# Kernel tuning notes

Measured on AMD Instinct MI355X. Metric: run time of the kernel, lower is better.

The kernel has to match this reference:

```python
import jax, jax.numpy as jnp
import numpy as np

B, C, H, W = 32, 1024, 28, 28
TEXT_DIM = 768
ATTN_DIM = 256
REDUCTION = 16
RED = max(1, C // REDUCTION)


def setup_inputs() -> dict:
    key = jax.random.key(0)
    ks = jax.random.split(key, 8)
    x = jax.random.normal(ks[0], (B, C, H, W), dtype=jnp.float32)
    text_feat = jax.random.normal(ks[1], (B, TEXT_DIM), dtype=jnp.float32)
    # ChannelAttention shared MLP (Linear weights, torch layout [out, in], no bias)
    w1 = jax.random.normal(ks[2], (RED, C), dtype=jnp.float32) * (1.0 / np.sqrt(C))
    w2 = jax.random.normal(ks[3], (C, RED), dtype=jnp.float32) * (1.0 / np.sqrt(RED))
    # TextGuidedSpatialAttention projections
    wq = jax.random.normal(ks[4], (ATTN_DIM, TEXT_DIM), dtype=jnp.float32) * 0.001
    wk = jax.random.normal(ks[5], (ATTN_DIM, C), dtype=jnp.float32) * np.sqrt(2.0 / ATTN_DIM)
    wv = jax.random.normal(ks[6], (ATTN_DIM, C), dtype=jnp.float32) * np.sqrt(2.0 / ATTN_DIM)
    wo = jax.random.normal(ks[7], (1, ATTN_DIM), dtype=jnp.float32) * np.sqrt(2.0)
    return {"x": x, "text_feat": text_feat, "w1": w1, "w2": w2,
            "wq": wq, "wk": wk, "wv": wv, "wo": wo}


def _forward(x, text_feat, w1, w2, wq, wk, wv, wo):
    b, c, h, w = x.shape
    # ----- Channel attention -----
    avg = jnp.mean(x, axis=(2, 3))          # [B, C]
    mx = jnp.max(x, axis=(2, 3))            # [B, C]
    def mlp(z):
        return jax.nn.relu(z @ w1.T) @ w2.T  # [B, C]
    ch_attn = jax.nn.sigmoid(mlp(avg) + mlp(mx))   # [B, C]
    x = x * ch_attn[:, :, None, None]
    # ----- Text-guided spatial attention -----
    q = text_feat @ wq.T                     # [B, A]
    # 1x1 conv == channel contraction
    k = jnp.einsum('ac,bchw->bahw', wk, x).reshape(b, ATTN_DIM, h * w)  # [B, A, N]
    v = jnp.einsum('ac,bchw->bahw', wv, x).reshape(b, ATTN_DIM, h * w)  # [B, A, N]
    scores = jnp.einsum('ba,ban->bn', q, k) / jnp.sqrt(jnp.float32(ATTN_DIM))  # [B, N]
    attn_weights = jax.nn.softmax(scores, axis=-1)                      # [B, N]
    attended = jnp.einsum('bn,ban->ba', attn_weights, v)                # [B, A]
    # out_proj 1x1 conv on a spatially-constant tensor == scalar per batch, broadcast
    spatial_scalar = jax.nn.sigmoid(attended @ wo.T)                    # [B, 1]
    spatial_attn = jnp.broadcast_to(spatial_scalar[:, :, None, None], (b, 1, h, w))
    return x * spatial_attn, spatial_attn


def reference(x, text_feat, w1, w2, wq, wk, wv, wo):
    return _forward(x, text_feat, w1, w2, wq, wk, wv, wo)
```

## Files before the change

kernel.cpp:

```cpp
#include <hip/hip_runtime.h>
#include <math.h>

#define B_   32
#define C_   1024
#define N_   784
#define NF4  196
#define TD   768
#define AD   256
#define RED_ 64
#define OUT0 25690112
#define ROWS (B_*C_)
#define CH_  16
#define CPB  64

#define OFF_AVG  0
#define OFF_MAX  32768
#define OFF_CA   65536
#define OFF_Q    98304
#define OFF_HS   106496
#define OFF_WVO  108544
#define OFF_SV   109568
#define OFF_CNT  109600
#define OFF_PS   109632
#define OFF_PY   511040

__global__ void k_avgmax(const float* __restrict__ x, float* __restrict__ avg,
                         float* __restrict__ mx) {
    int wave = threadIdx.x >> 6, lane = threadIdx.x & 63;
    int row0 = blockIdx.x * 8 + wave * 2;
    const float4* r0 = (const float4*)(x + (size_t)row0 * N_);
    const float4* r1 = r0 + NF4;
    float s0 = 0.f, s1 = 0.f, m0 = -3.4e38f, m1 = -3.4e38f;
    #pragma unroll
    for (int j = 0; j < 3; ++j) {
        int i = lane + 64 * j;
        float4 v0 = r0[i], v1 = r1[i];
        s0 += v0.x + v0.y + v0.z + v0.w;
        s1 += v1.x + v1.y + v1.z + v1.w;
        m0 = fmaxf(m0, fmaxf(fmaxf(v0.x, v0.y), fmaxf(v0.z, v0.w)));
        m1 = fmaxf(m1, fmaxf(fmaxf(v1.x, v1.y), fmaxf(v1.z, v1.w)));
    }
    if (lane < 4) {
        float4 v0 = r0[192 + lane], v1 = r1[192 + lane];
        s0 += v0.x + v0.y + v0.z + v0.w;
        s1 += v1.x + v1.y + v1.z + v1.w;
        m0 = fmaxf(m0, fmaxf(fmaxf(v0.x, v0.y), fmaxf(v0.z, v0.w)));
        m1 = fmaxf(m1, fmaxf(fmaxf(v1.x, v1.y), fmaxf(v1.z, v1.w)));
    }
    for (int o = 32; o; o >>= 1) {
        s0 += __shfl_down(s0, o, 64);
        s1 += __shfl_down(s1, o, 64);
        m0 = fmaxf(m0, __shfl_down(m0, o, 64));
        m1 = fmaxf(m1, __shfl_down(m1, o, 64));
    }
    if (lane == 0) {
        avg[row0]     = s0 * (1.f / (float)N_); mx[row0]     = m0;
        avg[row0 + 1] = s1 * (1.f / (float)N_); mx[row0 + 1] = m1;
    }
}

__global__ void k_proj(const float* __restrict__ text, const float* __restrict__ wq,
                       const float* __restrict__ avg, const float* __restrict__ mx,
                       const float* __restrict__ w1, const float* __restrict__ wv,
                       const float* __restrict__ wo, float* __restrict__ q,
                       float* __restrict__ hs, float* __restrict__ wvo,
                       int* __restrict__ cnt) {
    int blk  = blockIdx.x;
    int wave = threadIdx.x >> 6, lane = threadIdx.x & 63;
    __shared__ float red[256];
    if (blk < 2048) {
        int w = blk * 4 + wave;
        int b = w >> 8, a = w & 255;
        const float4* tb = (const float4*)(text + (size_t)b * TD);
        const float4* wr = (const float4*)(wq + (size_t)a * TD);
        float acc = 0.f;
        #pragma unroll
        for (int j = 0; j < 3; ++j) {
            int i = lane + 64 * j;
            float4 tv = tb[i], wvv = wr[i];
            acc += tv.x * wvv.x + tv.y * wvv.y + tv.z * wvv.z + tv.w * wvv.w;
        }
        for (int o = 32; o; o >>= 1) acc += __shfl_down(acc, o, 64);
        if (lane == 0) q[(size_t)b * AD + a] = acc;
    } else if (blk < 2560) {
        int w = (blk - 2048) * 4 + wave;
        int b = w >> 6, r = w & 63;
        const float4* av = (const float4*)(avg + (size_t)b * C_);
        const float4* mv = (const float4*)(mx + (size_t)b * C_);
        const float4* wr = (const float4*)(w1 + (size_t)r * C_);
        float aa = 0.f, am = 0.f;
        #pragma unroll
        for (int j = 0; j < 4; ++j) {
            int i = lane + 64 * j;
            float4 wvv = wr[i], a4 = av[i], m4 = mv[i];
            aa += wvv.x * a4.x + wvv.y * a4.y + wvv.z * a4.z + wvv.w * a4.w;
            am += wvv.x * m4.x + wvv.y * m4.y + wvv.z * m4.z + wvv.w * m4.w;
        }
        for (int o = 32; o; o >>= 1) {
            aa += __shfl_down(aa, o, 64);
            am += __shfl_down(am, o, 64);
        }
        if (lane == 0) hs[(size_t)b * RED_ + r] = fmaxf(aa, 0.f) + fmaxf(am, 0.f);
    } else if (blk < 2576) {
        int local = blk - 2560;
        int t = threadIdx.x;
        int cl = t & 63, sl = t >> 6;
        int c = local * 64 + cl;
        const float* wvp = wv + (size_t)(sl * 64) * C_ + c;
        float acc = 0.f;
        #pragma unroll 8
        for (int a = 0; a < 64; ++a) acc += wo[sl * 64 + a] * wvp[(size_t)a * C_];
        red[t] = acc;
        __syncthreads();
        if (t < 64) wvo[local * 64 + t] = red[t] + red[64 + t] + red[128 + t] + red[192 + t];
    } else {
        if (threadIdx.x < B_) cnt[threadIdx.x] = 0;
    }
}

__global__ __launch_bounds__(256) void k_scores(
        const float* __restrict__ x, const float* __restrict__ q,
        const float* __restrict__ hs, const float* __restrict__ w2,
        const float* __restrict__ wk, const float* __restrict__ wvo,
        float* __restrict__ ca, float* __restrict__ partS, float* __restrict__ partY,
        int* __restrict__ cnt, float* __restrict__ sv) {
    int chunk = blockIdx.x, b = blockIdx.y, t = threadIdx.x;
    int wave = t >> 6, lane = t & 63;
    __shared__ float qs[AD];
    __shared__ float hss[RED_];
    __shared__ float redA[256], redB[256];
    __shared__ float gsg[CPB], gsh[CPB];
    __shared__ float4 l4s[4 * NF4], l4y[4 * NF4];
    __shared__ float rm[4], rs[4], rd[4];
    __shared__ int winflag;

    qs[t] = q[(size_t)b * AD + t];
    if (t < RED_) hss[t] = hs[(size_t)b * RED_ + t];
    __syncthreads();
    {
        int cl = t & 63, sl = t >> 6;
        int c  = chunk * CPB + cl;
        const float* wkp = wk + (size_t)(sl * 64) * C_ + c;
        float a2 = 0.f;
        #pragma unroll 8
        for (int a = 0; a < 64; ++a) a2 += qs[sl * 64 + a] * wkp[(size_t)a * C_];
        redA[t] = a2;
        const float* w2p = w2 + (size_t)c * RED_ + sl * 16;
        float a1 = 0.f;
        #pragma unroll
        for (int r = 0; r < 16; ++r) a1 += hss[sl * 16 + r] * w2p[r];
        redB[t] = a1;
    }
    __syncthreads();
    if (t < CPB) {
        float s2 = redA[t] + redA[64 + t] + redA[128 + t] + redA[192 + t];
        float s1 = redB[t] + redB[64 + t] + redB[128 + t] + redB[192 + t];
        float cav = 1.f / (1.f + __expf(-s1));
        ca[(size_t)b * C_ + chunk * CPB + t] = cav;
        gsg[t] = s2 * cav * 0.0625f;
        gsh[t] = wvo[chunk * CPB + t] * cav;
    }
    __syncthreads();
    const float4* xb4 = (const float4*)(x +
        ((size_t)b * C_ + (size_t)chunk * CPB + (size_t)wave * 16) * N_);
    float4 z = make_float4(0.f, 0.f, 0.f, 0.f);
    float4 s0 = z, s1v = z, s2v = z, s3 = z;
    float4 y0 = z, y1 = z, y2 = z, y3 = z;
    #pragma unroll 4
    for (int cc = 0; cc < 16; ++cc) {
        float gv = gsg[wave * 16 + cc], hv = gsh[wave * 16 + cc];
        const float4* row = xb4 + (size_t)cc * NF4;
        float4 v;
        v = row[lane];
        s0.x += gv*v.x; s0.y += gv*v.y; s0.z += gv*v.z; s0.w += gv*v.w;
        y0.x += hv*v.x; y0.y += hv*v.y; y0.z += hv*v.z; y0.w += hv*v.w;
        v = row[lane + 64];
        s1v.x += gv*v.x; s1v.y += gv*v.y; s1v.z += gv*v.z; s1v.w += gv*v.w;
        y1.x  += hv*v.x; y1.y  += hv*v.y; y1.z  += hv*v.z; y1.w  += hv*v.w;
        v = row[lane + 128];
        s2v.x += gv*v.x; s2v.y += gv*v.y; s2v.z += gv*v.z; s2v.w += gv*v.w;
        y2.x  += hv*v.x; y2.y  += hv*v.y; y2.z  += hv*v.z; y2.w  += hv*v.w;
        if (lane < 4) {
            v = row[lane + 192];
            s3.x += gv*v.x; s3.y += gv*v.y; s3.z += gv*v.z; s3.w += gv*v.w;
            y3.x += hv*v.x; y3.y += hv*v.y; y3.z += hv*v.z; y3.w += hv*v.w;
        }
    }
    l4s[wave * NF4 + lane]       = s0;
    l4s[wave * NF4 + lane + 64]  = s1v;
    l4s[wave * NF4 + lane + 128] = s2v;
    l4y[wave * NF4 + lane]       = y0;
    l4y[wave * NF4 + lane + 64]  = y1;
    l4y[wave * NF4 + lane + 128] = y2;
    if (lane < 4) {
        l4s[wave * NF4 + lane + 192] = s3;
        l4y[wave * NF4 + lane + 192] = y3;
    }
    __syncthreads();
    if (t < NF4) {
        float4 a = l4s[t], bb = l4s[NF4 + t], c4 = l4s[2 * NF4 + t], d = l4s[3 * NF4 + t];
        float4 r;
        r.x = a.x + bb.x + c4.x + d.x; r.y = a.y + bb.y + c4.y + d.y;
        r.z = a.z + bb.z + c4.z + d.z; r.w = a.w + bb.w + c4.w + d.w;
        ((float4*)(partS + ((size_t)b * CH_ + chunk) * N_))[t] = r;
        a = l4y[t]; bb = l4y[NF4 + t]; c4 = l4y[2 * NF4 + t]; d = l4y[3 * NF4 + t];
        r.x = a.x + bb.x + c4.x + d.x; r.y = a.y + bb.y + c4.y + d.y;
        r.z = a.z + bb.z + c4.z + d.z; r.w = a.w + bb.w + c4.w + d.w;
        ((float4*)(partY + ((size_t)b * CH_ + chunk) * N_))[t] = r;
    }
    __syncthreads();
    if (t == 0) {
        __threadfence();
        winflag = (atomicAdd(&cnt[b], 1) == CH_ - 1) ? 1 : 0;
    }
    __syncthreads();
    if (!winflag) return;
    __threadfence();
    const float* pS = partS + (size_t)b * CH_ * N_;
    const float* pY = partY + (size_t)b * CH_ * N_;
    float v0 = 0.f, v1 = 0.f, v2 = 0.f, v3 = 0.f;
    float w0 = 0.f, w1v = 0.f, w2v = 0.f, w3 = 0.f;
    for (int ch = 0; ch < CH_; ++ch) {
        const float* pcs = pS + (size_t)ch * N_;
        const float* pcy = pY + (size_t)ch * N_;
        v0 += pcs[t]; v1 += pcs[t + 256]; v2 += pcs[t + 512];
        w0 += pcy[t]; w1v += pcy[t + 256]; w2v += pcy[t + 512];
        if (t < 16) { v3 += pcs[t + 768]; w3 += pcy[t + 768]; }
    }
    float m = fmaxf(fmaxf(v0, v1), v2);
    if (t < 16) m = fmaxf(m, v3);
    for (int o = 32; o; o >>= 1) m = fmaxf(m, __shfl_down(m, o, 64));
    if (lane == 0) rm[wave] = m;
    __syncthreads();
    float M = fmaxf(fmaxf(rm[0], rm[1]), fmaxf(rm[2], rm[3]));
    float e0 = __expf(v0 - M), e1 = __expf(v1 - M), e2 = __expf(v2 - M);
    float e3 = (t < 16) ? __expf(v3 - M) : 0.f;
    float ssum = e0 + e1 + e2 + e3;
    float dot  = e0 * w0 + e1 * w1v + e2 * w2v + e3 * w3;
    for (int o = 32; o; o >>= 1) {
        ssum += __shfl_down(ssum, o, 64);
        dot  += __shfl_down(dot,  o, 64);
    }
    if (lane == 0) { rs[wave] = ssum; rd[wave] = dot; }
    __syncthreads();
    if (t == 0) {
        float S = rs[0] + rs[1] + rs[2] + rs[3];
        float D = rd[0] + rd[1] + rd[2] + rd[3];
        sv[b] = 1.f / (1.f + __expf(-D / S));
    }
}

__global__ void k_finalize(const float* __restrict__ x, const float* __restrict__ chattn,
                           const float* __restrict__ s, float* __restrict__ out) {
    int blk = blockIdx.x;
    if (blk < ROWS / 8) {
        int wave = threadIdx.x >> 6, lane = threadIdx.x & 63;
        int row0 = blk * 8 + wave * 2;
        int b    = row0 >> 10;
        float sb  = s[b];
        float sc0 = chattn[row0] * sb;
        float sc1 = chattn[row0 + 1] * sb;
        const float4* r0 = (const float4*)(x + (size_t)row0 * N_);
        const float4* r1 = r0 + NF4;
        float4* o0 = (float4*)(out + (size_t)row0 * N_);
        float4* o1 = o0 + NF4;
        #pragma unroll
        for (int j = 0; j < 3; ++j) {
            int i = lane + 64 * j;
            float4 v0 = r0[i], v1 = r1[i];
            v0.x *= sc0; v0.y *= sc0; v0.z *= sc0; v0.w *= sc0;
            v1.x *= sc1; v1.y *= sc1; v1.z *= sc1; v1.w *= sc1;
            o0[i] = v0; o1[i] = v1;
        }
        if (lane < 4) {
            int i = 192 + lane;
            float4 v0 = r0[i], v1 = r1[i];
            v0.x *= sc0; v0.y *= sc0; v0.z *= sc0; v0.w *= sc0;
            v1.x *= sc1; v1.y *= sc1; v1.z *= sc1; v1.w *= sc1;
            o0[i] = v0; o1[i] = v1;
        }
    } else {
        int idx = (blk - ROWS / 8) * 256 + threadIdx.x;
        if (idx < (B_ * N_) / 4) {
            int b = idx / (N_ / 4);
            float v = s[b];
            ((float4*)(out + OUT0))[idx] = make_float4(v, v, v, v);
        }
    }
}

extern "C" void kernel_launch(void* const* d_in, const int* in_sizes, int n_in,
                              void* d_out, int out_size, void* d_ws, size_t ws_size,
                              hipStream_t stream) {
    const float* x    = (const float*)d_in[0];
    const float* text = (const float*)d_in[1];
    const float* w1   = (const float*)d_in[2];
    const float* w2   = (const float*)d_in[3];
    const float* wq   = (const float*)d_in[4];
    const float* wk   = (const float*)d_in[5];
    const float* wv   = (const float*)d_in[6];
    const float* wo   = (const float*)d_in[7];
    float* out = (float*)d_out;
    float* ws  = (float*)d_ws;

    float* avg   = ws + OFF_AVG;
    float* mx    = ws + OFF_MAX;
    float* ca    = ws + OFF_CA;
    float* q     = ws + OFF_Q;
    float* hs    = ws + OFF_HS;
    float* wvo   = ws + OFF_WVO;
    float* sv    = ws + OFF_SV;
    int*   cnt   = (int*)(ws + OFF_CNT);
    float* partS = ws + OFF_PS;
    float* partY = ws + OFF_PY;

    k_avgmax<<<ROWS / 8, 256, 0, stream>>>(x, avg, mx);
    k_proj<<<2577, 256, 0, stream>>>(text, wq, avg, mx, w1, wv, wo, q, hs, wvo, cnt);
    k_scores<<<dim3(CH_, B_), 256, 0, stream>>>(x, q, hs, w2, wk, wvo, ca, partS, partY, cnt, sv);
    k_finalize<<<ROWS / 8 + 25, 256, 0, stream>>>(x, ca, sv, out);
}
```

Measured before the change: 266.7 us.

## Rebalance pipeline stages, precompute q·Wk per batch, halve channels per scores block

Moves the q projection and counter reset into the avg/max kernel so they overlap with the big reduction pass. The per-channel q·Wk contraction leaves the scores kernel and becomes its own stage in k_proj, written to a new workspace buffer gq. The scores grid doubles to 32 chunks of 32 channels so more blocks share the x pass. The finalize kernel now uses nontemporal stores for the output. The costs are an extra workspace round trip for gq and more partial results for the scores reduction to combine.

```diff
diff --git a/kernel.cpp b/kernel.cpp
--- a/kernel.cpp
+++ b/kernel.cpp
@@ -10,8 +10,10 @@
 #define RED_ 64
 #define OUT0 25690112
 #define ROWS (B_*C_)
-#define CH_  16
-#define CPB  64
+#define CH_  32
+#define CPB  32
+
+typedef float f4 __attribute__((ext_vector_type(4)));
 
 #define OFF_AVG  0
 #define OFF_MAX  32768
@@ -19,57 +21,51 @@
 #define OFF_Q    98304
 #define OFF_HS   106496
 #define OFF_WVO  108544
-#define OFF_SV   109568
-#define OFF_CNT  109600
-#define OFF_PS   109632
-#define OFF_PY   511040
-
-__global__ void k_avgmax(const float* __restrict__ x, float* __restrict__ avg,
-                         float* __restrict__ mx) {
+#define OFF_GQ   109568
+#define OFF_SV   142336
+#define OFF_CNT  142368
+#define OFF_PS   142400
+#define OFF_PY   945216
+
+__global__ void k_avgmax(const float* __restrict__ x, const float* __restrict__ text,
+                         const float* __restrict__ wq, float* __restrict__ avg,
+                         float* __restrict__ mx, float* __restrict__ q,
+                         int* __restrict__ cnt) {
+    int blk = blockIdx.x;
     int wave = threadIdx.x >> 6, lane = threadIdx.x & 63;
-    int row0 = blockIdx.x * 8 + wave * 2;
-    const float4* r0 = (const float4*)(x + (size_t)row0 * N_);
-    const float4* r1 = r0 + NF4;
-    float s0 = 0.f, s1 = 0.f, m0 = -3.4e38f, m1 = -3.4e38f;
-    #pragma unroll
-    for (int j = 0; j < 3; ++j) {
-        int i = lane + 64 * j;
-        float4 v0 = r0[i], v1 = r1[i];
-        s0 += v0.x + v0.y + v0.z + v0.w;
-        s1 += v1.x + v1.y + v1.z + v1.w;
-        m0 = fmaxf(m0, fmaxf(fmaxf(v0.x, v0.y), fmaxf(v0.z, v0.w)));
-        m1 = fmaxf(m1, fmaxf(fmaxf(v1.x, v1.y), fmaxf(v1.z, v1.w)));
-    }
-    if (lane < 4) {
-        float4 v0 = r0[192 + lane], v1 = r1[192 + lane];
-        s0 += v0.x + v0.y + v0.z + v0.w;
-        s1 += v1.x + v1.y + v1.z + v1.w;
-        m0 = fmaxf(m0, fmaxf(fmaxf(v0.x, v0.y), fmaxf(v0.z, v0.w)));
-        m1 = fmaxf(m1, fmaxf(fmaxf(v1.x, v1.y), fmaxf(v1.z, v1.w)));
-    }
-    for (int o = 32; o; o >>= 1) {
-        s0 += __shfl_down(s0, o, 64);
-        s1 += __shfl_down(s1, o, 64);
-        m0 = fmaxf(m0, __shfl_down(m0, o, 64));
-        m1 = fmaxf(m1, __shfl_down(m1, o, 64));
-    }
-    if (lane == 0) {
-        avg[row0]     = s0 * (1.f / (float)N_); mx[row0]     = m0;
-        avg[row0 + 1] = s1 * (1.f / (float)N_); mx[row0 + 1] = m1;
-    }
-}
-
-__global__ void k_proj(const float* __restrict__ text, const float* __restrict__ wq,
-                       const float* __restrict__ avg, const float* __restrict__ mx,
-                       const float* __restrict__ w1, const float* __restrict__ wv,
-                       const float* __restrict__ wo, float* __restrict__ q,
-                       float* __restrict__ hs, float* __restrict__ wvo,
-                       int* __restrict__ cnt) {
-    int blk  = blockIdx.x;
-    int wave = threadIdx.x >> 6, lane = threadIdx.x & 63;
-    __shared__ float red[256];
-    if (blk < 2048) {
-        int w = blk * 4 + wave;
+    if (blk < 4096) {
+        int row0 = blk * 8 + wave * 2;
+        const float4* r0 = (const float4*)(x + (size_t)row0 * N_);
+        const float4* r1 = r0 + NF4;
+        float s0 = 0.f, s1 = 0.f, m0 = -3.4e38f, m1 = -3.4e38f;
+        #pragma unroll
+        for (int j = 0; j < 3; ++j) {
+            int i = lane + 64 * j;
+            float4 v0 = r0[i], v1 = r1[i];
+            s0 += v0.x + v0.y + v0.z + v0.w;
+            s1 += v1.x + v1.y + v1.z + v1.w;
+            m0 = fmaxf(m0, fmaxf(fmaxf(v0.x, v0.y), fmaxf(v0.z, v0.w)));
+            m1 = fmaxf(m1, fmaxf(fmaxf(v1.x, v1.y), fmaxf(v1.z, v1.w)));
+        }
+        if (lane < 4) {
+            float4 v0 = r0[192 + lane], v1 = r1[192 + lane];
+            s0 += v0.x + v0.y + v0.z + v0.w;
+            s1 += v1.x + v1.y + v1.z + v1.w;
+            m0 = fmaxf(m0, fmaxf(fmaxf(v0.x, v0.y), fmaxf(v0.z, v0.w)));
+            m1 = fmaxf(m1, fmaxf(fmaxf(v1.x, v1.y), fmaxf(v1.z, v1.w)));
+        }
+        for (int o = 32; o; o >>= 1) {
+            s0 += __shfl_down(s0, o, 64);
+            s1 += __shfl_down(s1, o, 64);
+            m0 = fmaxf(m0, __shfl_down(m0, o, 64));
+            m1 = fmaxf(m1, __shfl_down(m1, o, 64));
+        }
+        if (lane == 0) {
+            avg[row0]     = s0 * (1.f / (float)N_); mx[row0]     = m0;
+            avg[row0 + 1] = s1 * (1.f / (float)N_); mx[row0 + 1] = m1;
+        }
+    } else if (blk < 6144) {
+        int w = (blk - 4096) * 4 + wave;
         int b = w >> 8, a = w & 255;
         const float4* tb = (const float4*)(text + (size_t)b * TD);
         const float4* wr = (const float4*)(wq + (size_t)a * TD);
@@ -82,8 +78,23 @@
         }
         for (int o = 32; o; o >>= 1) acc += __shfl_down(acc, o, 64);
         if (lane == 0) q[(size_t)b * AD + a] = acc;
-    } else if (blk < 2560) {
-        int w = (blk - 2048) * 4 + wave;
+    } else {
+        if (threadIdx.x < B_) cnt[threadIdx.x] = 0;
+    }
+}
+
+__global__ void k_proj(const float* __restrict__ avg, const float* __restrict__ mx,
+                       const float* __restrict__ w1, const float* __restrict__ q,
+                       const float* __restrict__ wk, const float* __restrict__ wv,
+                       const float* __restrict__ wo, float* __restrict__ hs,
+                       float* __restrict__ gq, float* __restrict__ wvo) {
+    int blk  = blockIdx.x;
+    int wave = threadIdx.x >> 6, lane = threadIdx.x & 63;
+    int t = threadIdx.x;
+    __shared__ float red[256];
+    __shared__ float qs[AD];
+    if (blk < 512) {
+        int w = blk * 4 + wave;
         int b = w >> 6, r = w & 63;
         const float4* av = (const float4*)(avg + (size_t)b * C_);
         const float4* mv = (const float4*)(mx + (size_t)b * C_);
@@ -101,9 +112,22 @@
             am += __shfl_down(am, o, 64);
         }
         if (lane == 0) hs[(size_t)b * RED_ + r] = fmaxf(aa, 0.f) + fmaxf(am, 0.f);
-    } else if (blk < 2576) {
-        int local = blk - 2560;
-        int t = threadIdx.x;
+    } else if (blk < 1024) {
+        int local = blk - 512;
+        int b  = local >> 4, cb = local & 15;
+        int cl = t & 63, sl = t >> 6;
+        int c  = cb * 64 + cl;
+        qs[t] = q[(size_t)b * AD + t];
+        __syncthreads();
+        const float* wkp = wk + (size_t)(sl * 64) * C_ + c;
+        float acc = 0.f;
+        #pragma unroll 8
+        for (int a = 0; a < 64; ++a) acc += qs[sl * 64 + a] * wkp[(size_t)a * C_];
+        red[t] = acc;
+        __syncthreads();
+        if (t < 64) gq[(size_t)b * C_ + c] = red[t] + red[64 + t] + red[128 + t] + red[192 + t];
+    } else {
+        int local = blk - 1024;
         int cl = t & 63, sl = t >> 6;
         int c = local * 64 + cl;
         const float* wvp = wv + (size_t)(sl * 64) * C_ + c;
@@ -113,62 +137,55 @@
         red[t] = acc;
         __syncthreads();
         if (t < 64) wvo[local * 64 + t] = red[t] + red[64 + t] + red[128 + t] + red[192 + t];
-    } else {
-        if (threadIdx.x < B_) cnt[threadIdx.x] = 0;
     }
 }
 
 __global__ __launch_bounds__(256) void k_scores(
-        const float* __restrict__ x, const float* __restrict__ q,
-        const float* __restrict__ hs, const float* __restrict__ w2,
-        const float* __restrict__ wk, const float* __restrict__ wvo,
+        const float* __restrict__ x, const float* __restrict__ hs,
+        const float* __restrict__ w2, const float* __restrict__ gq,
+        const float* __restrict__ wvo,
         float* __restrict__ ca, float* __restrict__ partS, float* __restrict__ partY,
         int* __restrict__ cnt, float* __restrict__ sv) {
     int chunk = blockIdx.x, b = blockIdx.y, t = threadIdx.x;
     int wave = t >> 6, lane = t & 63;
-    __shared__ float qs[AD];
     __shared__ float hss[RED_];
-    __shared__ float redA[256], redB[256];
+    __shared__ float redB[256];
     __shared__ float gsg[CPB], gsh[CPB];
     __shared__ float4 l4s[4 * NF4], l4y[4 * NF4];
     __shared__ float rm[4], rs[4], rd[4];
     __shared__ int winflag;
 
-    qs[t] = q[(size_t)b * AD + t];
     if (t < RED_) hss[t] = hs[(size_t)b * RED_ + t];
     __syncthreads();
     {
-        int cl = t & 63, sl = t >> 6;
+        int cl = t & 31, sl = t >> 5;
         int c  = chunk * CPB + cl;
-        const float* wkp = wk + (size_t)(sl * 64) * C_ + c;
-        float a2 = 0.f;
-        #pragma unroll 8
-        for (int a = 0; a < 64; ++a) a2 += qs[sl * 64 + a] * wkp[(size_t)a * C_];
-        redA[t] = a2;
-        const float* w2p = w2 + (size_t)c * RED_ + sl * 16;
+        const float* w2p = w2 + (size_t)c * RED_ + sl * 8;
         float a1 = 0.f;
         #pragma unroll
-        for (int r = 0; r < 16; ++r) a1 += hss[sl * 16 + r] * w2p[r];
+        for (int r = 0; r < 8; ++r) a1 += hss[sl * 8 + r] * w2p[r];
         redB[t] = a1;
     }
     __syncthreads();
     if (t < CPB) {
-        float s2 = redA[t] + redA[64 + t] + redA[128 + t] + redA[192 + t];
-        float s1 = redB[t] + redB[64 + t] + redB[128 + t] + redB[192 + t];
+        float s1 = 0.f;
+        #pragma unroll
+        for (int k = 0; k < 8; ++k) s1 += redB[k * 32 + t];
         float cav = 1.f / (1.f + __expf(-s1));
-        ca[(size_t)b * C_ + chunk * CPB + t] = cav;
-        gsg[t] = s2 * cav * 0.0625f;
-        gsh[t] = wvo[chunk * CPB + t] * cav;
+        int c = chunk * CPB + t;
+        ca[(size_t)b * C_ + c] = cav;
+        gsg[t] = gq[(size_t)b * C_ + c] * cav * 0.0625f;
+        gsh[t] = wvo[c] * cav;
     }
     __syncthreads();
     const float4* xb4 = (const float4*)(x +
-        ((size_t)b * C_ + (size_t)chunk * CPB + (size_t)wave * 16) * N_);
+        ((size_t)b * C_ + (size_t)chunk * CPB + (size_t)wave * 8) * N_);
     float4 z = make_float4(0.f, 0.f, 0.f, 0.f);
     float4 s0 = z, s1v = z, s2v = z, s3 = z;
     float4 y0 = z, y1 = z, y2 = z, y3 = z;
     #pragma unroll 4
-    for (int cc = 0; cc < 16; ++cc) {
-        float gv = gsg[wave * 16 + cc], hv = gsh[wave * 16 + cc];
+    for (int cc = 0; cc < 8; ++cc) {
+        float gv = gsg[wave * 8 + cc], hv = gsh[wave * 8 + cc];
         const float4* row = xb4 + (size_t)cc * NF4;
         float4 v;
         v = row[lane];
@@ -262,29 +279,32 @@
         float sc1 = chattn[row0 + 1] * sb;
         const float4* r0 = (const float4*)(x + (size_t)row0 * N_);
         const float4* r1 = r0 + NF4;
-        float4* o0 = (float4*)(out + (size_t)row0 * N_);
-        float4* o1 = o0 + NF4;
+        f4* o0 = (f4*)(out + (size_t)row0 * N_);
+        f4* o1 = o0 + NF4;
         #pragma unroll
         for (int j = 0; j < 3; ++j) {
             int i = lane + 64 * j;
             float4 v0 = r0[i], v1 = r1[i];
-            v0.x *= sc0; v0.y *= sc0; v0.z *= sc0; v0.w *= sc0;
-            v1.x *= sc1; v1.y *= sc1; v1.z *= sc1; v1.w *= sc1;
-            o0[i] = v0; o1[i] = v1;
+            f4 w0 = { v0.x * sc0, v0.y * sc0, v0.z * sc0, v0.w * sc0 };
+            f4 w1 = { v1.x * sc1, v1.y * sc1, v1.z * sc1, v1.w * sc1 };
+            __builtin_nontemporal_store(w0, &o0[i]);
+            __builtin_nontemporal_store(w1, &o1[i]);
         }
         if (lane < 4) {
             int i = 192 + lane;
             float4 v0 = r0[i], v1 = r1[i];
-            v0.x *= sc0; v0.y *= sc0; v0.z *= sc0; v0.w *= sc0;
-            v1.x *= sc1; v1.y *= sc1; v1.z *= sc1; v1.w *= sc1;
-            o0[i] = v0; o1[i] = v1;
+            f4 w0 = { v0.x * sc0, v0.y * sc0, v0.z * sc0, v0.w * sc0 };
+            f4 w1 = { v1.x * sc1, v1.y * sc1, v1.z * sc1, v1.w * sc1 };
+            __builtin_nontemporal_store(w0, &o0[i]);
+            __builtin_nontemporal_store(w1, &o1[i]);
         }
     } else {
         int idx = (blk - ROWS / 8) * 256 + threadIdx.x;
         if (idx < (B_ * N_) / 4) {
             int b = idx / (N_ / 4);
             float v = s[b];
-            ((float4*)(out + OUT0))[idx] = make_float4(v, v, v, v);
+            f4 vv = { v, v, v, v };
+            __builtin_nontemporal_store(vv, &((f4*)(out + OUT0))[idx]);
         }
     }
 }
@@ -309,13 +329,14 @@
     float* q     = ws + OFF_Q;
     float* hs    = ws + OFF_HS;
     float* wvo   = ws + OFF_WVO;
+    float* gq    = ws + OFF_GQ;
     float* sv    = ws + OFF_SV;
     int*   cnt   = (int*)(ws + OFF_CNT);
     float* partS = ws + OFF_PS;
     float* partY = ws + OFF_PY;
 
-    k_avgmax<<<ROWS / 8, 256, 0, stream>>>(x, avg, mx);
-    k_proj<<<2577, 256, 0, stream>>>(text, wq, avg, mx, w1, wv, wo, q, hs, wvo, cnt);
-    k_scores<<<dim3(CH_, B_), 256, 0, stream>>>(x, q, hs, w2, wk, wvo, ca, partS, partY, cnt, sv);
+    k_avgmax<<<6145, 256, 0, stream>>>(x, text, wq, avg, mx, q, cnt);
+    k_proj<<<1040, 256, 0, stream>>>(avg, mx, w1, q, wk, wv, wo, hs, gq, wvo);
+    k_scores<<<dim3(CH_, B_), 256, 0, stream>>>(x, hs, w2, gq, wvo, ca, partS, partY, cnt, sv);
     k_finalize<<<ROWS / 8 + 25, 256, 0, stream>>>(x, ca, sv, out);
 }
```

After: 286.7 us. 7.5% more time.
